# Kernel optimization log

Measured on AMD Instinct MI355X. Metric: run time of the kernel, lower is better.

Reference implementation:

```python
import jax, jax.numpy as jnp
import numpy as np

# Model constants (match init_kwargs)
B, S, H = 32, 1, 128          # batch, query seq len (decode), num query heads
SKV, G = 8192, 1              # KV cache length, KV groups (heads per group = H // G)
DIM, TAIL = 512, 64           # MLA latent (value) dim and RoPE tail dim
TOPK = 2048                   # selected KV tokens per (query, group)
KV_STRIDE = 1                 # tokens covered per KV entry
Q_START = 8191                # absolute position of the first query token
SCALE = 1.0 / np.sqrt(DIM + TAIL)  # sm_scale default: 1/sqrt(qk head dim)
NEG_INF = -1e30


def setup_inputs() -> dict:
    key = jax.random.key(0)
    kq, kkv, ki = jax.random.split(key, 3)
    Q = jax.random.normal(kq, (B, S, H, DIM + TAIL), dtype=jnp.float32)
    KV = jax.random.normal(kkv, (B, SKV, G, DIM + TAIL), dtype=jnp.float32)
    Indices = jnp.sort(
        jax.random.randint(ki, (B, S, G, TOPK), 0, SKV, dtype=jnp.int32), axis=-1)
    return {"Q": Q, "KV": KV, "Indices": Indices}


def reference(Q, KV, Indices):
    Hg = H // G  # query heads per KV group
    # Gather top-k selected KV latents: kv_sel[b,s,g,k,:] = KV[b, Indices[b,s,g,k], g, :]
    b_idx = jnp.arange(B)[:, None, None, None]
    g_idx = jnp.arange(G)[None, None, :, None]
    kv_sel = KV[b_idx, Indices, g_idx, :]               # [B, S, G, K, DIM+TAIL]
    q = Q.reshape(B, S, G, Hg, DIM + TAIL)              # group the query heads
    # Attention scores over the k selected tokens only (full dim+tail qk dot)
    scores = jnp.einsum('bsghd,bsgkd->bsghk', q, kv_sel) * SCALE
    # Causal validity: selected KV token (covering KV_STRIDE positions) must not
    # exceed the absolute query position Q_START + s.
    q_pos = Q_START + jnp.arange(S)                     # [S]
    valid = (Indices * KV_STRIDE <= q_pos[None, :, None, None]) & (Indices < SKV)
    scores = jnp.where(valid[:, :, :, None, :], scores, NEG_INF)
    p = jax.nn.softmax(scores, axis=-1)                 # [B, S, G, Hg, K]
    # Values are the first DIM channels of the latent KV (MLA: V shares latent)
    out = jnp.einsum('bsghk,bsgkd->bsghd', p, kv_sel[..., :DIM])
    return out.reshape(B, S, H, DIM)
```

## Files before the change

kernel.cpp:

```cpp
#include <hip/hip_runtime.h>
#include <hip/hip_bf16.h>

typedef short bf16x8 __attribute__((ext_vector_type(8)));
typedef float f32x4  __attribute__((ext_vector_type(4)));

#define NB    32
#define NH    128
#define DV    512
#define DQK   576
#define NKV   8192
#define NTOP  2048
#define LSTR  40
#define SCALE 0.041666666666666664f

__device__ __forceinline__ unsigned bfbits(float x) {
  union { float f; unsigned u; } c; c.f = x;
  return (c.u + 0x7FFFu + ((c.u >> 16) & 1u)) >> 16;
}
__device__ __forceinline__ unsigned pk2(float x, float y) {
  return bfbits(x) | (bfbits(y) << 16);
}
__device__ __forceinline__ short f2bf(float x) {
  return (short)bfbits(x);
}

__global__ __launch_bounds__(256) void gemm_qk(const float* __restrict__ Q, const float* __restrict__ KV,
                                               const int* __restrict__ Idx, float* __restrict__ S) {
  __shared__ short As[128 * LSTR];
  __shared__ short Bs[128 * LSTR];
  int wg = blockIdx.x;
  int b = wg >> 4, nt = wg & 15;
  int t = threadIdx.x;

  int row2 = t >> 1, half = t & 1;
  int idx = Idx[b * NTOP + nt * 128 + row2];
  const float* kvrow = KV + ((size_t)b * NKV + (size_t)idx) * DQK + half * 16;
  const float* qrow  = Q  + ((size_t)b * NH  + (size_t)row2) * DQK + half * 16;
  short* aw = &As[row2 * LSTR + half * 16];
  short* bw = &Bs[row2 * LSTR + half * 16];

  int lane = t & 63, wv = t >> 6;
  int wm = wv & 1, wn = wv >> 1;
  int m16 = lane & 15, quad = lane >> 4;

  f32x4 acc[4][4] = {};

  for (int kk = 0; kk < 18; ++kk) {
    __syncthreads();
    float4 q0 = *(const float4*)(qrow + 0);
    float4 q1 = *(const float4*)(qrow + 4);
    float4 q2 = *(const float4*)(qrow + 8);
    float4 q3 = *(const float4*)(qrow + 12);
    float4 k0 = *(const float4*)(kvrow + 0);
    float4 k1 = *(const float4*)(kvrow + 4);
    float4 k2 = *(const float4*)(kvrow + 8);
    float4 k3 = *(const float4*)(kvrow + 12);
    int4 wa0 = { (int)pk2(q0.x, q0.y), (int)pk2(q0.z, q0.w), (int)pk2(q1.x, q1.y), (int)pk2(q1.z, q1.w) };
    int4 wa1 = { (int)pk2(q2.x, q2.y), (int)pk2(q2.z, q2.w), (int)pk2(q3.x, q3.y), (int)pk2(q3.z, q3.w) };
    int4 wb0 = { (int)pk2(k0.x, k0.y), (int)pk2(k0.z, k0.w), (int)pk2(k1.x, k1.y), (int)pk2(k1.z, k1.w) };
    int4 wb1 = { (int)pk2(k2.x, k2.y), (int)pk2(k2.z, k2.w), (int)pk2(k3.x, k3.y), (int)pk2(k3.z, k3.w) };
    *(int4*)aw = wa0; *(int4*)(aw + 8) = wa1;
    *(int4*)bw = wb0; *(int4*)(bw + 8) = wb1;
    qrow += 32; kvrow += 32;
    __syncthreads();

    bf16x8 af[4], bfr[4];
#pragma unroll
    for (int i = 0; i < 4; ++i) af[i]  = *(const bf16x8*)&As[(wm * 64 + i * 16 + m16) * LSTR + quad * 8];
#pragma unroll
    for (int j = 0; j < 4; ++j) bfr[j] = *(const bf16x8*)&Bs[(wn * 64 + j * 16 + m16) * LSTR + quad * 8];
#pragma unroll
    for (int i = 0; i < 4; ++i)
#pragma unroll
      for (int j = 0; j < 4; ++j)
        acc[i][j] = __builtin_amdgcn_mfma_f32_16x16x32_bf16(af[i], bfr[j], acc[i][j], 0, 0, 0);
  }

#pragma unroll
  for (int i = 0; i < 4; ++i)
#pragma unroll
    for (int j = 0; j < 4; ++j)
#pragma unroll
      for (int r = 0; r < 4; ++r) {
        int h = wm * 64 + i * 16 + quad * 4 + r;
        int n = nt * 128 + wn * 64 + j * 16 + m16;
        S[((size_t)b * NH + h) * NTOP + n] = acc[i][j][r] * SCALE;
      }
}

__global__ __launch_bounds__(256) void softmax_k(const float* __restrict__ S, unsigned short* __restrict__ P) {
  int row = blockIdx.x;
  const float* s = S + (size_t)row * NTOP;
  unsigned short* p = P + (size_t)row * NTOP;
  int t = threadIdx.x;
  int lane = t & 63, wv = t >> 6;
  __shared__ float red[4];

  float4 v0 = *(const float4*)(s + t * 4);
  float4 v1 = *(const float4*)(s + 1024 + t * 4);

  float lm = fmaxf(fmaxf(fmaxf(v0.x, v0.y), fmaxf(v0.z, v0.w)),
                   fmaxf(fmaxf(v1.x, v1.y), fmaxf(v1.z, v1.w)));
  for (int off = 32; off > 0; off >>= 1) lm = fmaxf(lm, __shfl_down(lm, off));
  if (lane == 0) red[wv] = lm;
  __syncthreads();
  float m = fmaxf(fmaxf(red[0], red[1]), fmaxf(red[2], red[3]));

  float e0 = expf(v0.x - m), e1 = expf(v0.y - m), e2 = expf(v0.z - m), e3 = expf(v0.w - m);
  float e4 = expf(v1.x - m), e5 = expf(v1.y - m), e6 = expf(v1.z - m), e7 = expf(v1.w - m);
  float ls = ((e0 + e1) + (e2 + e3)) + ((e4 + e5) + (e6 + e7));
  for (int off = 32; off > 0; off >>= 1) ls += __shfl_down(ls, off);
  __syncthreads();
  if (lane == 0) red[wv] = ls;
  __syncthreads();
  float inv = 1.0f / (((red[0] + red[1]) + (red[2] + red[3])));

  uint2 o0 = { pk2(e0 * inv, e1 * inv), pk2(e2 * inv, e3 * inv) };
  uint2 o1 = { pk2(e4 * inv, e5 * inv), pk2(e6 * inv, e7 * inv) };
  *(uint2*)(p + t * 4) = o0;
  *(uint2*)(p + 1024 + t * 4) = o1;
}

__global__ __launch_bounds__(256) void gemm_pv(const unsigned short* __restrict__ P, const float* __restrict__ KV,
                                               const int* __restrict__ Idx, float* __restrict__ Out) {
  __shared__ short As[128 * LSTR];
  __shared__ short Bt[128 * LSTR];
  int wg = blockIdx.x;
  int b = wg >> 4, nt = (wg >> 2) & 3, ks = wg & 3;
  int t = threadIdx.x;

  int arow = t >> 1, ahalf = t & 1;
  const unsigned short* prow = P + ((size_t)b * NH + arow) * NTOP + ks * 512 + ahalf * 16;
  short* aw = &As[arow * LSTR + ahalf * 16];

  int brow = t & 31;
  int bcol = (t >> 5) * 16;
  const int* idxp = Idx + b * NTOP + ks * 512 + brow;
  short* bw = &Bt[bcol * LSTR + brow];

  int lane = t & 63, wv = t >> 6;
  int wm = wv & 1, wn = wv >> 1;
  int m16 = lane & 15, quad = lane >> 4;

  f32x4 acc[4][4] = {};

  for (int kk = 0; kk < 16; ++kk) {
    __syncthreads();
    uint4 p0 = *(const uint4*)(prow);
    uint4 p1 = *(const uint4*)(prow + 8);
    int idx = idxp[kk * 32];
    const float* vrow = KV + ((size_t)b * NKV + (size_t)idx) * DQK + nt * 128 + bcol;
    float4 v0 = *(const float4*)(vrow + 0);
    float4 v1 = *(const float4*)(vrow + 4);
    float4 v2 = *(const float4*)(vrow + 8);
    float4 v3 = *(const float4*)(vrow + 12);
    *(uint4*)aw = p0; *(uint4*)(aw + 8) = p1;
    prow += 32;
    bw[0 * LSTR]  = f2bf(v0.x); bw[1 * LSTR]  = f2bf(v0.y); bw[2 * LSTR]  = f2bf(v0.z); bw[3 * LSTR]  = f2bf(v0.w);
    bw[4 * LSTR]  = f2bf(v1.x); bw[5 * LSTR]  = f2bf(v1.y); bw[6 * LSTR]  = f2bf(v1.z); bw[7 * LSTR]  = f2bf(v1.w);
    bw[8 * LSTR]  = f2bf(v2.x); bw[9 * LSTR]  = f2bf(v2.y); bw[10 * LSTR] = f2bf(v2.z); bw[11 * LSTR] = f2bf(v2.w);
    bw[12 * LSTR] = f2bf(v3.x); bw[13 * LSTR] = f2bf(v3.y); bw[14 * LSTR] = f2bf(v3.z); bw[15 * LSTR] = f2bf(v3.w);
    __syncthreads();

    bf16x8 af[4], bfr[4];
#pragma unroll
    for (int i = 0; i < 4; ++i) af[i]  = *(const bf16x8*)&As[(wm * 64 + i * 16 + m16) * LSTR + quad * 8];
#pragma unroll
    for (int j = 0; j < 4; ++j) bfr[j] = *(const bf16x8*)&Bt[(wn * 64 + j * 16 + m16) * LSTR + quad * 8];
#pragma unroll
    for (int i = 0; i < 4; ++i)
#pragma unroll
      for (int j = 0; j < 4; ++j)
        acc[i][j] = __builtin_amdgcn_mfma_f32_16x16x32_bf16(af[i], bfr[j], acc[i][j], 0, 0, 0);
  }

#pragma unroll
  for (int i = 0; i < 4; ++i)
#pragma unroll
    for (int j = 0; j < 4; ++j)
#pragma unroll
      for (int r = 0; r < 4; ++r) {
        int h = wm * 64 + i * 16 + quad * 4 + r;
        int d = nt * 128 + wn * 64 + j * 16 + m16;
        atomicAdd(&Out[((size_t)b * NH + h) * DV + d], acc[i][j][r]);
      }
}

extern "C" void kernel_launch(void* const* d_in, const int* in_sizes, int n_in,
                              void* d_out, int out_size, void* d_ws, size_t ws_size,
                              hipStream_t stream) {
  const float* Q  = (const float*)d_in[0];
  const float* KV = (const float*)d_in[1];
  const int*  Idx = (const int*)d_in[2];

  float* S = (float*)d_ws;
  unsigned short* P = (unsigned short*)((char*)d_ws + (size_t)NB * NH * NTOP * 4);
  float* Out = (float*)d_out;

  (void)hipMemsetAsync(d_out, 0, (size_t)out_size * sizeof(float), stream);
  gemm_qk<<<dim3(NB * 16), dim3(256), 0, stream>>>(Q, KV, Idx, S);
  softmax_k<<<dim3(NB * NH), dim3(256), 0, stream>>>(S, P);
  gemm_pv<<<dim3(NB * 16), dim3(256), 0, stream>>>(P, KV, Idx, Out);
}
```

Before: 738.3 us.

## Pre-gather KV into bf16 K and transposed V, share one pipelined GEMM

Adds a gather-and-convert kernel that pulls the top-k KV rows once, converts them to bf16 and writes both a row-major K buffer and a transposed V buffer. Q is converted to bf16 separately. Both GEMMs then use a single templated bf16 NT GEMM with register prefetch of the next k-slice, replacing the fp32 loads, in-loop conversions and scalar transposed LDS stores. The PV split-K atomics are replaced by per-split partial outputs plus a reduction kernel. This adds extra workspace traffic and two more launches in exchange for contiguous, already-converted operand loads.

```diff
diff --git a/kernel.cpp b/kernel.cpp
--- a/kernel.cpp
+++ b/kernel.cpp
@@ -1,8 +1,8 @@
 #include <hip/hip_runtime.h>
-#include <hip/hip_bf16.h>
 
 typedef short bf16x8 __attribute__((ext_vector_type(8)));
 typedef float f32x4  __attribute__((ext_vector_type(4)));
+typedef unsigned short u16;
 
 #define NB    32
 #define NH    128
@@ -10,8 +10,14 @@
 #define DQK   576
 #define NKV   8192
 #define NTOP  2048
-#define LSTR  40
 #define SCALE 0.041666666666666664f
+
+#define OFF_S   0u
+#define OFF_P   33554432u
+#define OFF_QB  50331648u
+#define OFF_KB  55050240u
+#define OFF_VT  130547712u
+#define OFF_OP  197656576u
 
 __device__ __forceinline__ unsigned bfbits(float x) {
   union { float f; unsigned u; } c; c.f = x;
@@ -20,55 +26,136 @@
 __device__ __forceinline__ unsigned pk2(float x, float y) {
   return bfbits(x) | (bfbits(y) << 16);
 }
-__device__ __forceinline__ short f2bf(float x) {
-  return (short)bfbits(x);
-}
-
-__global__ __launch_bounds__(256) void gemm_qk(const float* __restrict__ Q, const float* __restrict__ KV,
-                                               const int* __restrict__ Idx, float* __restrict__ S) {
-  __shared__ short As[128 * LSTR];
-  __shared__ short Bs[128 * LSTR];
-  int wg = blockIdx.x;
-  int b = wg >> 4, nt = wg & 15;
+
+__global__ __launch_bounds__(256) void cvt_q(const float* __restrict__ Q, u16* __restrict__ Qb) {
+  int i = (blockIdx.x * 256 + threadIdx.x) * 8;
+  float4 a = *(const float4*)(Q + i), b = *(const float4*)(Q + i + 4);
+  uint4 o = { pk2(a.x, a.y), pk2(a.z, a.w), pk2(b.x, b.y), pk2(b.z, b.w) };
+  *(uint4*)(Qb + i) = o;
+}
+
+__global__ __launch_bounds__(256) void gather_cvt(const float* __restrict__ KV, const int* __restrict__ Idx,
+                                                  u16* __restrict__ Kb, u16* __restrict__ Vt) {
+  __shared__ u16 T[128 * 136];
+  int nt = blockIdx.x, b = blockIdx.y;
+  int j0 = nt * 128;
   int t = threadIdx.x;
-
-  int row2 = t >> 1, half = t & 1;
-  int idx = Idx[b * NTOP + nt * 128 + row2];
-  const float* kvrow = KV + ((size_t)b * NKV + (size_t)idx) * DQK + half * 16;
-  const float* qrow  = Q  + ((size_t)b * NH  + (size_t)row2) * DQK + half * 16;
-  short* aw = &As[row2 * LSTR + half * 16];
-  short* bw = &Bs[row2 * LSTR + half * 16];
+  const int* idxp = Idx + b * NTOP + j0;
+  const float* KVb = KV + (size_t)b * NKV * DQK;
+  u16* Kbb = Kb + ((size_t)b * NTOP + j0) * DQK;
+
+  int kq = (t & 31) * 4, dq = (t >> 5) * 16;
+  int4 id4 = *(const int4*)&idxp[kq];
+  const float* r0 = KVb + (size_t)id4.x * DQK + dq;
+  const float* r1 = KVb + (size_t)id4.y * DQK + dq;
+  const float* r2 = KVb + (size_t)id4.z * DQK + dq;
+  const float* r3 = KVb + (size_t)id4.w * DQK + dq;
+
+  int sd = t >> 1, skh = (t & 1) * 64;
+
+  for (int c = 0; c < 4; ++c) {
+    int co = c * 128;
+    unsigned rr[4][16];
+#pragma unroll
+    for (int i = 0; i < 4; ++i) {
+      const float* rp = (i == 0) ? r0 : (i == 1) ? r1 : (i == 2) ? r2 : r3;
+      float4 x0 = *(const float4*)(rp + co + 0);
+      float4 x1 = *(const float4*)(rp + co + 4);
+      float4 x2 = *(const float4*)(rp + co + 8);
+      float4 x3 = *(const float4*)(rp + co + 12);
+      rr[i][0] = bfbits(x0.x); rr[i][1] = bfbits(x0.y); rr[i][2]  = bfbits(x0.z); rr[i][3]  = bfbits(x0.w);
+      rr[i][4] = bfbits(x1.x); rr[i][5] = bfbits(x1.y); rr[i][6]  = bfbits(x1.z); rr[i][7]  = bfbits(x1.w);
+      rr[i][8] = bfbits(x2.x); rr[i][9] = bfbits(x2.y); rr[i][10] = bfbits(x2.z); rr[i][11] = bfbits(x2.w);
+      rr[i][12] = bfbits(x3.x); rr[i][13] = bfbits(x3.y); rr[i][14] = bfbits(x3.z); rr[i][15] = bfbits(x3.w);
+    }
+#pragma unroll
+    for (int i = 0; i < 4; ++i) {
+      uint4 w0 = { rr[i][0] | (rr[i][1] << 16), rr[i][2] | (rr[i][3] << 16),
+                   rr[i][4] | (rr[i][5] << 16), rr[i][6] | (rr[i][7] << 16) };
+      uint4 w1 = { rr[i][8] | (rr[i][9] << 16), rr[i][10] | (rr[i][11] << 16),
+                   rr[i][12] | (rr[i][13] << 16), rr[i][14] | (rr[i][15] << 16) };
+      u16* kp = Kbb + (size_t)(kq + i) * DQK + co + dq;
+      *(uint4*)kp = w0; *(uint4*)(kp + 8) = w1;
+    }
+#pragma unroll
+    for (int i2 = 0; i2 < 16; ++i2) {
+      uint2 w = { rr[0][i2] | (rr[1][i2] << 16), rr[2][i2] | (rr[3][i2] << 16) };
+      *(uint2*)&T[(dq + i2) * 136 + kq] = w;
+    }
+    __syncthreads();
+    u16* vp = Vt + ((size_t)b * DV + co + sd) * NTOP + j0 + skh;
+    const u16* tp = &T[sd * 136 + skh];
+#pragma unroll
+    for (int c2 = 0; c2 < 8; ++c2)
+      *(uint4*)(vp + c2 * 8) = *(const uint4*)(tp + c2 * 8);
+    __syncthreads();
+  }
+
+  int row = t >> 1, half = t & 1;
+  int idx = idxp[row];
+  const float* src = KVb + (size_t)idx * DQK + 512 + half * 32;
+  u16* dst = Kbb + (size_t)row * DQK + 512 + half * 32;
+  unsigned u[16];
+#pragma unroll
+  for (int q = 0; q < 8; ++q) {
+    float4 x = *(const float4*)(src + q * 4);
+    u[q * 2] = pk2(x.x, x.y); u[q * 2 + 1] = pk2(x.z, x.w);
+  }
+#pragma unroll
+  for (int q = 0; q < 4; ++q) {
+    uint4 w = { u[q * 4], u[q * 4 + 1], u[q * 4 + 2], u[q * 4 + 3] };
+    *(uint4*)(dst + q * 8) = w;
+  }
+}
+
+template <int NKI, int LD>
+__global__ __launch_bounds__(256) void gemm_nt(const u16* __restrict__ A, const u16* __restrict__ B,
+                                               float* __restrict__ C, int ldc,
+                                               int aB, int bB, int bT, int cB, int cT, int cK, int KS,
+                                               float scale) {
+  __shared__ u16 As[128 * 32];
+  __shared__ u16 Bs[128 * 32];
+  int nt = blockIdx.x, b = blockIdx.y, ks = blockIdx.z;
+  const u16* Ab = A + (size_t)b * aB + (size_t)ks * KS;
+  const u16* Bb = B + (size_t)b * bB + (size_t)nt * bT + (size_t)ks * KS;
+  float* Cb = C + (size_t)b * cB + (size_t)nt * cT + (size_t)ks * cK;
+
+  int t = threadIdx.x;
+  int r0 = t >> 2, kq = (t & 3) * 8;
+  const u16* ag = Ab + (size_t)r0 * LD + kq;
+  const u16* bg = Bb + (size_t)r0 * LD + kq;
+  u16* aw = &As[r0 * 32 + kq];
+  u16* bw = &Bs[r0 * 32 + kq];
 
   int lane = t & 63, wv = t >> 6;
   int wm = wv & 1, wn = wv >> 1;
   int m16 = lane & 15, quad = lane >> 4;
 
+  uint4 ra0 = *(const uint4*)(ag);
+  uint4 ra1 = *(const uint4*)(ag + (size_t)64 * LD);
+  uint4 rb0 = *(const uint4*)(bg);
+  uint4 rb1 = *(const uint4*)(bg + (size_t)64 * LD);
+
   f32x4 acc[4][4] = {};
 
-  for (int kk = 0; kk < 18; ++kk) {
-    __syncthreads();
-    float4 q0 = *(const float4*)(qrow + 0);
-    float4 q1 = *(const float4*)(qrow + 4);
-    float4 q2 = *(const float4*)(qrow + 8);
-    float4 q3 = *(const float4*)(qrow + 12);
-    float4 k0 = *(const float4*)(kvrow + 0);
-    float4 k1 = *(const float4*)(kvrow + 4);
-    float4 k2 = *(const float4*)(kvrow + 8);
-    float4 k3 = *(const float4*)(kvrow + 12);
-    int4 wa0 = { (int)pk2(q0.x, q0.y), (int)pk2(q0.z, q0.w), (int)pk2(q1.x, q1.y), (int)pk2(q1.z, q1.w) };
-    int4 wa1 = { (int)pk2(q2.x, q2.y), (int)pk2(q2.z, q2.w), (int)pk2(q3.x, q3.y), (int)pk2(q3.z, q3.w) };
-    int4 wb0 = { (int)pk2(k0.x, k0.y), (int)pk2(k0.z, k0.w), (int)pk2(k1.x, k1.y), (int)pk2(k1.z, k1.w) };
-    int4 wb1 = { (int)pk2(k2.x, k2.y), (int)pk2(k2.z, k2.w), (int)pk2(k3.x, k3.y), (int)pk2(k3.z, k3.w) };
-    *(int4*)aw = wa0; *(int4*)(aw + 8) = wa1;
-    *(int4*)bw = wb0; *(int4*)(bw + 8) = wb1;
-    qrow += 32; kvrow += 32;
-    __syncthreads();
-
+  for (int kk = 0; kk < NKI; ++kk) {
+    __syncthreads();
+    *(uint4*)aw = ra0; *(uint4*)(aw + 64 * 32) = ra1;
+    *(uint4*)bw = rb0; *(uint4*)(bw + 64 * 32) = rb1;
+    __syncthreads();
+    if (kk + 1 < NKI) {
+      const u16* an = ag + (kk + 1) * 32;
+      const u16* bn = bg + (kk + 1) * 32;
+      ra0 = *(const uint4*)(an);
+      ra1 = *(const uint4*)(an + (size_t)64 * LD);
+      rb0 = *(const uint4*)(bn);
+      rb1 = *(const uint4*)(bn + (size_t)64 * LD);
+    }
     bf16x8 af[4], bfr[4];
 #pragma unroll
-    for (int i = 0; i < 4; ++i) af[i]  = *(const bf16x8*)&As[(wm * 64 + i * 16 + m16) * LSTR + quad * 8];
-#pragma unroll
-    for (int j = 0; j < 4; ++j) bfr[j] = *(const bf16x8*)&Bs[(wn * 64 + j * 16 + m16) * LSTR + quad * 8];
+    for (int i = 0; i < 4; ++i) af[i]  = *(const bf16x8*)&As[(wm * 64 + i * 16 + m16) * 32 + quad * 8];
+#pragma unroll
+    for (int j = 0; j < 4; ++j) bfr[j] = *(const bf16x8*)&Bs[(wn * 64 + j * 16 + m16) * 32 + quad * 8];
 #pragma unroll
     for (int i = 0; i < 4; ++i)
 #pragma unroll
@@ -82,16 +169,16 @@
     for (int j = 0; j < 4; ++j)
 #pragma unroll
       for (int r = 0; r < 4; ++r) {
-        int h = wm * 64 + i * 16 + quad * 4 + r;
-        int n = nt * 128 + wn * 64 + j * 16 + m16;
-        S[((size_t)b * NH + h) * NTOP + n] = acc[i][j][r] * SCALE;
+        int m = wm * 64 + i * 16 + quad * 4 + r;
+        int n = wn * 64 + j * 16 + m16;
+        Cb[(size_t)m * ldc + n] = acc[i][j][r] * scale;
       }
 }
 
-__global__ __launch_bounds__(256) void softmax_k(const float* __restrict__ S, unsigned short* __restrict__ P) {
+__global__ __launch_bounds__(256) void softmax_k(const float* __restrict__ S, u16* __restrict__ P) {
   int row = blockIdx.x;
   const float* s = S + (size_t)row * NTOP;
-  unsigned short* p = P + (size_t)row * NTOP;
+  u16* p = P + (size_t)row * NTOP;
   int t = threadIdx.x;
   int lane = t & 63, wv = t >> 6;
   __shared__ float red[4];
@@ -121,69 +208,16 @@
   *(uint2*)(p + 1024 + t * 4) = o1;
 }
 
-__global__ __launch_bounds__(256) void gemm_pv(const unsigned short* __restrict__ P, const float* __restrict__ KV,
-                                               const int* __restrict__ Idx, float* __restrict__ Out) {
-  __shared__ short As[128 * LSTR];
-  __shared__ short Bt[128 * LSTR];
-  int wg = blockIdx.x;
-  int b = wg >> 4, nt = (wg >> 2) & 3, ks = wg & 3;
-  int t = threadIdx.x;
-
-  int arow = t >> 1, ahalf = t & 1;
-  const unsigned short* prow = P + ((size_t)b * NH + arow) * NTOP + ks * 512 + ahalf * 16;
-  short* aw = &As[arow * LSTR + ahalf * 16];
-
-  int brow = t & 31;
-  int bcol = (t >> 5) * 16;
-  const int* idxp = Idx + b * NTOP + ks * 512 + brow;
-  short* bw = &Bt[bcol * LSTR + brow];
-
-  int lane = t & 63, wv = t >> 6;
-  int wm = wv & 1, wn = wv >> 1;
-  int m16 = lane & 15, quad = lane >> 4;
-
-  f32x4 acc[4][4] = {};
-
-  for (int kk = 0; kk < 16; ++kk) {
-    __syncthreads();
-    uint4 p0 = *(const uint4*)(prow);
-    uint4 p1 = *(const uint4*)(prow + 8);
-    int idx = idxp[kk * 32];
-    const float* vrow = KV + ((size_t)b * NKV + (size_t)idx) * DQK + nt * 128 + bcol;
-    float4 v0 = *(const float4*)(vrow + 0);
-    float4 v1 = *(const float4*)(vrow + 4);
-    float4 v2 = *(const float4*)(vrow + 8);
-    float4 v3 = *(const float4*)(vrow + 12);
-    *(uint4*)aw = p0; *(uint4*)(aw + 8) = p1;
-    prow += 32;
-    bw[0 * LSTR]  = f2bf(v0.x); bw[1 * LSTR]  = f2bf(v0.y); bw[2 * LSTR]  = f2bf(v0.z); bw[3 * LSTR]  = f2bf(v0.w);
-    bw[4 * LSTR]  = f2bf(v1.x); bw[5 * LSTR]  = f2bf(v1.y); bw[6 * LSTR]  = f2bf(v1.z); bw[7 * LSTR]  = f2bf(v1.w);
-    bw[8 * LSTR]  = f2bf(v2.x); bw[9 * LSTR]  = f2bf(v2.y); bw[10 * LSTR] = f2bf(v2.z); bw[11 * LSTR] = f2bf(v2.w);
-    bw[12 * LSTR] = f2bf(v3.x); bw[13 * LSTR] = f2bf(v3.y); bw[14 * LSTR] = f2bf(v3.z); bw[15 * LSTR] = f2bf(v3.w);
-    __syncthreads();
-
-    bf16x8 af[4], bfr[4];
-#pragma unroll
-    for (int i = 0; i < 4; ++i) af[i]  = *(const bf16x8*)&As[(wm * 64 + i * 16 + m16) * LSTR + quad * 8];
-#pragma unroll
-    for (int j = 0; j < 4; ++j) bfr[j] = *(const bf16x8*)&Bt[(wn * 64 + j * 16 + m16) * LSTR + quad * 8];
-#pragma unroll
-    for (int i = 0; i < 4; ++i)
-#pragma unroll
-      for (int j = 0; j < 4; ++j)
-        acc[i][j] = __builtin_amdgcn_mfma_f32_16x16x32_bf16(af[i], bfr[j], acc[i][j], 0, 0, 0);
-  }
-
-#pragma unroll
-  for (int i = 0; i < 4; ++i)
-#pragma unroll
-    for (int j = 0; j < 4; ++j)
-#pragma unroll
-      for (int r = 0; r < 4; ++r) {
-        int h = wm * 64 + i * 16 + quad * 4 + r;
-        int d = nt * 128 + wn * 64 + j * 16 + m16;
-        atomicAdd(&Out[((size_t)b * NH + h) * DV + d], acc[i][j][r]);
-      }
+__global__ __launch_bounds__(256) void reduce4(const float* __restrict__ Op, float* __restrict__ Out) {
+  size_t i = ((size_t)blockIdx.x * 256 + threadIdx.x) * 4;
+  const size_t STRIDE = (size_t)NB * NH * DV;
+  float4 s0 = *(const float4*)(Op + i);
+  float4 s1 = *(const float4*)(Op + STRIDE + i);
+  float4 s2 = *(const float4*)(Op + 2 * STRIDE + i);
+  float4 s3 = *(const float4*)(Op + 3 * STRIDE + i);
+  float4 o = { (s0.x + s1.x) + (s2.x + s3.x), (s0.y + s1.y) + (s2.y + s3.y),
+               (s0.z + s1.z) + (s2.z + s3.z), (s0.w + s1.w) + (s2.w + s3.w) };
+  *(float4*)(Out + i) = o;
 }
 
 extern "C" void kernel_launch(void* const* d_in, const int* in_sizes, int n_in,
@@ -193,12 +227,25 @@
   const float* KV = (const float*)d_in[1];
   const int*  Idx = (const int*)d_in[2];
 
-  float* S = (float*)d_ws;
-  unsigned short* P = (unsigned short*)((char*)d_ws + (size_t)NB * NH * NTOP * 4);
+  char* ws = (char*)d_ws;
+  float* S   = (float*)(ws + OFF_S);
+  u16*   P   = (u16*)(ws + OFF_P);
+  u16*   Qb  = (u16*)(ws + OFF_QB);
+  u16*   Kb  = (u16*)(ws + OFF_KB);
+  u16*   Vt  = (u16*)(ws + OFF_VT);
+  float* Op  = (float*)(ws + OFF_OP);
   float* Out = (float*)d_out;
 
-  (void)hipMemsetAsync(d_out, 0, (size_t)out_size * sizeof(float), stream);
-  gemm_qk<<<dim3(NB * 16), dim3(256), 0, stream>>>(Q, KV, Idx, S);
+  cvt_q<<<dim3(1152), dim3(256), 0, stream>>>(Q, Qb);
+  gather_cvt<<<dim3(16, 32), dim3(256), 0, stream>>>(KV, Idx, Kb, Vt);
+  gemm_nt<18, 576><<<dim3(16, 32, 1), dim3(256), 0, stream>>>(
+      Qb, Kb, S, NTOP,
+       NH * DQK,  NTOP * DQK,  128 * DQK,
+       NH * NTOP,  128,  0,  0, SCALE);
   softmax_k<<<dim3(NB * NH), dim3(256), 0, stream>>>(S, P);
-  gemm_pv<<<dim3(NB * 16), dim3(256), 0, stream>>>(P, KV, Idx, Out);
-}
+  gemm_nt<16, 2048><<<dim3(4, 32, 4), dim3(256), 0, stream>>>(
+      P, Vt, Op, DV,
+       NH * NTOP,  DV * NTOP,  128 * NTOP,
+       NH * DV,  128,  NB * NH * DV,  512, 1.0f);
+  reduce4<<<dim3(2048), dim3(256), 0, stream>>>(Op, Out);
+}
```

Measured after the change: 788.7 us. 1.07x slower.

## Fuse QK, softmax and PV into split-K flash kernel with combine pass

Applied to the files above, without the earlier changes.

Replaces the three-kernel pipeline (QK GEMM to a global score matrix, separate softmax, PV GEMM with atomics) with one split-K flash-style kernel. Each block handles 128 selected keys: it computes scores, takes a local max/sum softmax into shared memory, and multiplies by gathered V, writing partial outputs plus row max and sum. A second kernel rescales and combines the 16 partials. This removes the fp32 score and P round-trips, the memset and the atomics, and adds register prefetch of the next QK tile and a swizzled V layout. In exchange it writes a large fp32 partial-output buffer (16x the output size) and adds a combine pass.

```diff
diff --git a/kernel.cpp b/kernel.cpp
--- a/kernel.cpp
+++ b/kernel.cpp
@@ -1,8 +1,8 @@
 #include <hip/hip_runtime.h>
-#include <hip/hip_bf16.h>
 
 typedef short bf16x8 __attribute__((ext_vector_type(8)));
 typedef float f32x4  __attribute__((ext_vector_type(4)));
+typedef unsigned short u16;
 
 #define NB    32
 #define NH    128
@@ -10,8 +10,14 @@
 #define DQK   576
 #define NKV   8192
 #define NTOP  2048
-#define LSTR  40
+#define NCH   16
+#define KC    128
+#define PSTR  136
 #define SCALE 0.041666666666666664f
+
+#define OFF_OP 0u
+#define OFF_M  134217728u
+#define OFF_L  134479872u
 
 __device__ __forceinline__ unsigned bfbits(float x) {
   union { float f; unsigned u; } c; c.f = x;
@@ -20,170 +26,245 @@
 __device__ __forceinline__ unsigned pk2(float x, float y) {
   return bfbits(x) | (bfbits(y) << 16);
 }
-__device__ __forceinline__ short f2bf(float x) {
-  return (short)bfbits(x);
-}
-
-__global__ __launch_bounds__(256) void gemm_qk(const float* __restrict__ Q, const float* __restrict__ KV,
-                                               const int* __restrict__ Idx, float* __restrict__ S) {
-  __shared__ short As[128 * LSTR];
-  __shared__ short Bs[128 * LSTR];
-  int wg = blockIdx.x;
-  int b = wg >> 4, nt = wg & 15;
+
+__global__ __launch_bounds__(256) void flash_chunk(const float* __restrict__ Q, const float* __restrict__ KV,
+                                                   const int* __restrict__ Idx,
+                                                   float* __restrict__ Op, float* __restrict__ Mg,
+                                                   float* __restrict__ Lg) {
+  __shared__ u16 Psh[128 * PSTR];
+  __shared__ u16 U[8192];
+  __shared__ float Msh[2 * 128];
+  __shared__ float Lsh[2 * 128];
+
+  u16* As = U;
+  u16* Bs = U + 4096;
+  u16* Vt = U;
+
+  int blk = blockIdx.x;
+  int b = blk >> 4, ks = blk & 15;
   int t = threadIdx.x;
-
-  int row2 = t >> 1, half = t & 1;
-  int idx = Idx[b * NTOP + nt * 128 + row2];
-  const float* kvrow = KV + ((size_t)b * NKV + (size_t)idx) * DQK + half * 16;
-  const float* qrow  = Q  + ((size_t)b * NH  + (size_t)row2) * DQK + half * 16;
-  short* aw = &As[row2 * LSTR + half * 16];
-  short* bw = &Bs[row2 * LSTR + half * 16];
-
   int lane = t & 63, wv = t >> 6;
   int wm = wv & 1, wn = wv >> 1;
   int m16 = lane & 15, quad = lane >> 4;
 
+  const float* Qb  = Q  + (size_t)b * NH * DQK;
+  const float* KVb = KV + (size_t)b * NKV * DQK;
+  const int* idxp  = Idx + b * NTOP + ks * KC;
+
+  int sr = t >> 1, sh = (t & 1) * 16;
+  int bidx = idxp[sr];
+  const float* aq = Qb + (size_t)sr * DQK + sh;
+  const float* bk = KVb + (size_t)bidx * DQK + sh;
+  u16* aw = &As[sr * 32 + sh];
+  u16* bw = &Bs[sr * 32 + sh];
+
   f32x4 acc[4][4] = {};
+
+  float4 a0 = *(const float4*)(aq);
+  float4 a1 = *(const float4*)(aq + 4);
+  float4 a2 = *(const float4*)(aq + 8);
+  float4 a3 = *(const float4*)(aq + 12);
+  float4 b0 = *(const float4*)(bk);
+  float4 b1 = *(const float4*)(bk + 4);
+  float4 b2 = *(const float4*)(bk + 8);
+  float4 b3 = *(const float4*)(bk + 12);
 
   for (int kk = 0; kk < 18; ++kk) {
     __syncthreads();
-    float4 q0 = *(const float4*)(qrow + 0);
-    float4 q1 = *(const float4*)(qrow + 4);
-    float4 q2 = *(const float4*)(qrow + 8);
-    float4 q3 = *(const float4*)(qrow + 12);
-    float4 k0 = *(const float4*)(kvrow + 0);
-    float4 k1 = *(const float4*)(kvrow + 4);
-    float4 k2 = *(const float4*)(kvrow + 8);
-    float4 k3 = *(const float4*)(kvrow + 12);
-    int4 wa0 = { (int)pk2(q0.x, q0.y), (int)pk2(q0.z, q0.w), (int)pk2(q1.x, q1.y), (int)pk2(q1.z, q1.w) };
-    int4 wa1 = { (int)pk2(q2.x, q2.y), (int)pk2(q2.z, q2.w), (int)pk2(q3.x, q3.y), (int)pk2(q3.z, q3.w) };
-    int4 wb0 = { (int)pk2(k0.x, k0.y), (int)pk2(k0.z, k0.w), (int)pk2(k1.x, k1.y), (int)pk2(k1.z, k1.w) };
-    int4 wb1 = { (int)pk2(k2.x, k2.y), (int)pk2(k2.z, k2.w), (int)pk2(k3.x, k3.y), (int)pk2(k3.z, k3.w) };
-    *(int4*)aw = wa0; *(int4*)(aw + 8) = wa1;
-    *(int4*)bw = wb0; *(int4*)(bw + 8) = wb1;
-    qrow += 32; kvrow += 32;
+    {
+      uint4 wa0 = { pk2(a0.x, a0.y), pk2(a0.z, a0.w), pk2(a1.x, a1.y), pk2(a1.z, a1.w) };
+      uint4 wa1 = { pk2(a2.x, a2.y), pk2(a2.z, a2.w), pk2(a3.x, a3.y), pk2(a3.z, a3.w) };
+      uint4 wb0 = { pk2(b0.x, b0.y), pk2(b0.z, b0.w), pk2(b1.x, b1.y), pk2(b1.z, b1.w) };
+      uint4 wb1 = { pk2(b2.x, b2.y), pk2(b2.z, b2.w), pk2(b3.x, b3.y), pk2(b3.z, b3.w) };
+      *(uint4*)aw = wa0; *(uint4*)(aw + 8) = wa1;
+      *(uint4*)bw = wb0; *(uint4*)(bw + 8) = wb1;
+    }
     __syncthreads();
-
-    bf16x8 af[4], bfr[4];
-#pragma unroll
-    for (int i = 0; i < 4; ++i) af[i]  = *(const bf16x8*)&As[(wm * 64 + i * 16 + m16) * LSTR + quad * 8];
-#pragma unroll
-    for (int j = 0; j < 4; ++j) bfr[j] = *(const bf16x8*)&Bs[(wn * 64 + j * 16 + m16) * LSTR + quad * 8];
+    if (kk + 1 < 18) {
+      const float* an = aq + (kk + 1) * 32;
+      const float* bn = bk + (kk + 1) * 32;
+      a0 = *(const float4*)(an);     a1 = *(const float4*)(an + 4);
+      a2 = *(const float4*)(an + 8); a3 = *(const float4*)(an + 12);
+      b0 = *(const float4*)(bn);     b1 = *(const float4*)(bn + 4);
+      b2 = *(const float4*)(bn + 8); b3 = *(const float4*)(bn + 12);
+    }
+    bf16x8 af[4], bf[4];
+#pragma unroll
+    for (int i = 0; i < 4; ++i) af[i] = *(const bf16x8*)&As[(wm * 64 + i * 16 + m16) * 32 + quad * 8];
+#pragma unroll
+    for (int j = 0; j < 4; ++j) bf[j] = *(const bf16x8*)&Bs[(wn * 64 + j * 16 + m16) * 32 + quad * 8];
 #pragma unroll
     for (int i = 0; i < 4; ++i)
 #pragma unroll
       for (int j = 0; j < 4; ++j)
-        acc[i][j] = __builtin_amdgcn_mfma_f32_16x16x32_bf16(af[i], bfr[j], acc[i][j], 0, 0, 0);
+        acc[i][j] = __builtin_amdgcn_mfma_f32_16x16x32_bf16(af[i], bf[j], acc[i][j], 0, 0, 0);
   }
 
 #pragma unroll
   for (int i = 0; i < 4; ++i)
 #pragma unroll
     for (int j = 0; j < 4; ++j)
+      acc[i][j] *= SCALE;
+
+  float mx[4][4];
+#pragma unroll
+  for (int i = 0; i < 4; ++i)
+#pragma unroll
+    for (int r = 0; r < 4; ++r) {
+      float v = fmaxf(fmaxf(acc[i][0][r], acc[i][1][r]), fmaxf(acc[i][2][r], acc[i][3][r]));
+      v = fmaxf(v, __shfl_xor(v, 1)); v = fmaxf(v, __shfl_xor(v, 2));
+      v = fmaxf(v, __shfl_xor(v, 4)); v = fmaxf(v, __shfl_xor(v, 8));
+      mx[i][r] = v;
+    }
+  if (m16 == 0) {
+#pragma unroll
+    for (int i = 0; i < 4; ++i)
+#pragma unroll
+      for (int r = 0; r < 4; ++r)
+        Msh[wn * 128 + wm * 64 + i * 16 + quad * 4 + r] = mx[i][r];
+  }
+  __syncthreads();
+  float mrw[4][4];
+#pragma unroll
+  for (int i = 0; i < 4; ++i)
+#pragma unroll
+    for (int r = 0; r < 4; ++r) {
+      int row = wm * 64 + i * 16 + quad * 4 + r;
+      mrw[i][r] = fmaxf(Msh[row], Msh[128 + row]);
+    }
+  float sm[4][4];
+#pragma unroll
+  for (int i = 0; i < 4; ++i)
+#pragma unroll
+    for (int r = 0; r < 4; ++r) {
+      float s = 0.f;
+#pragma unroll
+      for (int j = 0; j < 4; ++j) {
+        float e = expf(acc[i][j][r] - mrw[i][r]);
+        acc[i][j][r] = e;
+        s += e;
+      }
+      s += __shfl_xor(s, 1); s += __shfl_xor(s, 2);
+      s += __shfl_xor(s, 4); s += __shfl_xor(s, 8);
+      sm[i][r] = s;
+    }
+  if (m16 == 0) {
+#pragma unroll
+    for (int i = 0; i < 4; ++i)
+#pragma unroll
+      for (int r = 0; r < 4; ++r)
+        Lsh[wn * 128 + wm * 64 + i * 16 + quad * 4 + r] = sm[i][r];
+  }
+#pragma unroll
+  for (int i = 0; i < 4; ++i)
+#pragma unroll
+    for (int j = 0; j < 4; ++j)
 #pragma unroll
       for (int r = 0; r < 4; ++r) {
-        int h = wm * 64 + i * 16 + quad * 4 + r;
-        int n = nt * 128 + wn * 64 + j * 16 + m16;
-        S[((size_t)b * NH + h) * NTOP + n] = acc[i][j][r] * SCALE;
-      }
-}
-
-__global__ __launch_bounds__(256) void softmax_k(const float* __restrict__ S, unsigned short* __restrict__ P) {
+        int row = wm * 64 + i * 16 + quad * 4 + r;
+        int col = wn * 64 + j * 16 + m16;
+        Psh[row * PSTR + col] = (u16)bfbits(acc[i][j][r]);
+      }
+  __syncthreads();
+  if (wn == 0 && m16 == 0) {
+    float* mg = Mg + (b * NCH + ks) * NH;
+    float* lg = Lg + (b * NCH + ks) * NH;
+#pragma unroll
+    for (int i = 0; i < 4; ++i)
+#pragma unroll
+      for (int r = 0; r < 4; ++r) {
+        int row = wm * 64 + i * 16 + quad * 4 + r;
+        mg[row] = mrw[i][r];
+        lg[row] = Lsh[row] + Lsh[128 + row];
+      }
+  }
+
+  int p  = t & 15;
+  int dg = t >> 4;
+  float* opb = Op + (((size_t)ks * NB + b) * NH) * DV;
+
+  for (int dh = 0; dh < 4; ++dh) {
+    f32x4 a4[4][4] = {};
+    for (int k2 = 0; k2 < 4; ++k2) {
+      int key0 = k2 * 32 + p * 2;
+      int i0 = idxp[key0], i1 = idxp[key0 + 1];
+      const float* v0p = KVb + (size_t)i0 * DQK + dh * 128 + dg * 8;
+      const float* v1p = KVb + (size_t)i1 * DQK + dh * 128 + dg * 8;
+      float4 x0 = *(const float4*)(v0p);
+      float4 x1 = *(const float4*)(v0p + 4);
+      float4 y0 = *(const float4*)(v1p);
+      float4 y1 = *(const float4*)(v1p + 4);
+      unsigned lo[8] = { bfbits(x0.x), bfbits(x0.y), bfbits(x0.z), bfbits(x0.w),
+                         bfbits(x1.x), bfbits(x1.y), bfbits(x1.z), bfbits(x1.w) };
+      unsigned hi[8] = { bfbits(y0.x), bfbits(y0.y), bfbits(y0.z), bfbits(y0.w),
+                         bfbits(y1.x), bfbits(y1.y), bfbits(y1.z), bfbits(y1.w) };
+      __syncthreads();
+      int chunk = (p >> 2) ^ (dg & 3);
+#pragma unroll
+      for (int jj = 0; jj < 8; ++jj) {
+        int row = dg * 8 + jj;
+        int elem = row * 32 + chunk * 8 + (p & 3) * 2;
+        *(unsigned*)&Vt[elem] = lo[jj] | (hi[jj] << 16);
+      }
+      __syncthreads();
+      bf16x8 af2[4], bf2[4];
+#pragma unroll
+      for (int i = 0; i < 4; ++i)
+        af2[i] = *(const bf16x8*)&Psh[(wm * 64 + i * 16 + m16) * PSTR + k2 * 32 + quad * 8];
+#pragma unroll
+      for (int j = 0; j < 4; ++j) {
+        int row = wn * 64 + j * 16 + m16;
+        int rchunk = quad ^ ((row >> 3) & 3);
+        bf2[j] = *(const bf16x8*)&Vt[row * 32 + rchunk * 8];
+      }
+#pragma unroll
+      for (int i = 0; i < 4; ++i)
+#pragma unroll
+        for (int j = 0; j < 4; ++j)
+          a4[i][j] = __builtin_amdgcn_mfma_f32_16x16x32_bf16(af2[i], bf2[j], a4[i][j], 0, 0, 0);
+    }
+#pragma unroll
+    for (int i = 0; i < 4; ++i)
+#pragma unroll
+      for (int j = 0; j < 4; ++j)
+#pragma unroll
+        for (int r = 0; r < 4; ++r) {
+          int h = wm * 64 + i * 16 + quad * 4 + r;
+          int d = dh * 128 + wn * 64 + j * 16 + m16;
+          opb[(size_t)h * DV + d] = a4[i][j][r];
+        }
+  }
+}
+
+__global__ __launch_bounds__(256) void combine(const float* __restrict__ Op, const float* __restrict__ Mg,
+                                               const float* __restrict__ Lg, float* __restrict__ Out) {
   int row = blockIdx.x;
-  const float* s = S + (size_t)row * NTOP;
-  unsigned short* p = P + (size_t)row * NTOP;
+  int b = row >> 7, h = row & 127;
   int t = threadIdx.x;
-  int lane = t & 63, wv = t >> 6;
-  __shared__ float red[4];
-
-  float4 v0 = *(const float4*)(s + t * 4);
-  float4 v1 = *(const float4*)(s + 1024 + t * 4);
-
-  float lm = fmaxf(fmaxf(fmaxf(v0.x, v0.y), fmaxf(v0.z, v0.w)),
-                   fmaxf(fmaxf(v1.x, v1.y), fmaxf(v1.z, v1.w)));
-  for (int off = 32; off > 0; off >>= 1) lm = fmaxf(lm, __shfl_down(lm, off));
-  if (lane == 0) red[wv] = lm;
-  __syncthreads();
-  float m = fmaxf(fmaxf(red[0], red[1]), fmaxf(red[2], red[3]));
-
-  float e0 = expf(v0.x - m), e1 = expf(v0.y - m), e2 = expf(v0.z - m), e3 = expf(v0.w - m);
-  float e4 = expf(v1.x - m), e5 = expf(v1.y - m), e6 = expf(v1.z - m), e7 = expf(v1.w - m);
-  float ls = ((e0 + e1) + (e2 + e3)) + ((e4 + e5) + (e6 + e7));
-  for (int off = 32; off > 0; off >>= 1) ls += __shfl_down(ls, off);
-  __syncthreads();
-  if (lane == 0) red[wv] = ls;
-  __syncthreads();
-  float inv = 1.0f / (((red[0] + red[1]) + (red[2] + red[3])));
-
-  uint2 o0 = { pk2(e0 * inv, e1 * inv), pk2(e2 * inv, e3 * inv) };
-  uint2 o1 = { pk2(e4 * inv, e5 * inv), pk2(e6 * inv, e7 * inv) };
-  *(uint2*)(p + t * 4) = o0;
-  *(uint2*)(p + 1024 + t * 4) = o1;
-}
-
-__global__ __launch_bounds__(256) void gemm_pv(const unsigned short* __restrict__ P, const float* __restrict__ KV,
-                                               const int* __restrict__ Idx, float* __restrict__ Out) {
-  __shared__ short As[128 * LSTR];
-  __shared__ short Bt[128 * LSTR];
-  int wg = blockIdx.x;
-  int b = wg >> 4, nt = (wg >> 2) & 3, ks = wg & 3;
-  int t = threadIdx.x;
-
-  int arow = t >> 1, ahalf = t & 1;
-  const unsigned short* prow = P + ((size_t)b * NH + arow) * NTOP + ks * 512 + ahalf * 16;
-  short* aw = &As[arow * LSTR + ahalf * 16];
-
-  int brow = t & 31;
-  int bcol = (t >> 5) * 16;
-  const int* idxp = Idx + b * NTOP + ks * 512 + brow;
-  short* bw = &Bt[bcol * LSTR + brow];
-
-  int lane = t & 63, wv = t >> 6;
-  int wm = wv & 1, wn = wv >> 1;
-  int m16 = lane & 15, quad = lane >> 4;
-
-  f32x4 acc[4][4] = {};
-
-  for (int kk = 0; kk < 16; ++kk) {
-    __syncthreads();
-    uint4 p0 = *(const uint4*)(prow);
-    uint4 p1 = *(const uint4*)(prow + 8);
-    int idx = idxp[kk * 32];
-    const float* vrow = KV + ((size_t)b * NKV + (size_t)idx) * DQK + nt * 128 + bcol;
-    float4 v0 = *(const float4*)(vrow + 0);
-    float4 v1 = *(const float4*)(vrow + 4);
-    float4 v2 = *(const float4*)(vrow + 8);
-    float4 v3 = *(const float4*)(vrow + 12);
-    *(uint4*)aw = p0; *(uint4*)(aw + 8) = p1;
-    prow += 32;
-    bw[0 * LSTR]  = f2bf(v0.x); bw[1 * LSTR]  = f2bf(v0.y); bw[2 * LSTR]  = f2bf(v0.z); bw[3 * LSTR]  = f2bf(v0.w);
-    bw[4 * LSTR]  = f2bf(v1.x); bw[5 * LSTR]  = f2bf(v1.y); bw[6 * LSTR]  = f2bf(v1.z); bw[7 * LSTR]  = f2bf(v1.w);
-    bw[8 * LSTR]  = f2bf(v2.x); bw[9 * LSTR]  = f2bf(v2.y); bw[10 * LSTR] = f2bf(v2.z); bw[11 * LSTR] = f2bf(v2.w);
-    bw[12 * LSTR] = f2bf(v3.x); bw[13 * LSTR] = f2bf(v3.y); bw[14 * LSTR] = f2bf(v3.z); bw[15 * LSTR] = f2bf(v3.w);
-    __syncthreads();
-
-    bf16x8 af[4], bfr[4];
-#pragma unroll
-    for (int i = 0; i < 4; ++i) af[i]  = *(const bf16x8*)&As[(wm * 64 + i * 16 + m16) * LSTR + quad * 8];
-#pragma unroll
-    for (int j = 0; j < 4; ++j) bfr[j] = *(const bf16x8*)&Bt[(wn * 64 + j * 16 + m16) * LSTR + quad * 8];
-#pragma unroll
-    for (int i = 0; i < 4; ++i)
-#pragma unroll
-      for (int j = 0; j < 4; ++j)
-        acc[i][j] = __builtin_amdgcn_mfma_f32_16x16x32_bf16(af[i], bfr[j], acc[i][j], 0, 0, 0);
-  }
-
-#pragma unroll
-  for (int i = 0; i < 4; ++i)
-#pragma unroll
-    for (int j = 0; j < 4; ++j)
-#pragma unroll
-      for (int r = 0; r < 4; ++r) {
-        int h = wm * 64 + i * 16 + quad * 4 + r;
-        int d = nt * 128 + wn * 64 + j * 16 + m16;
-        atomicAdd(&Out[((size_t)b * NH + h) * DV + d], acc[i][j][r]);
-      }
+
+  float m[NCH], l[NCH];
+#pragma unroll
+  for (int c = 0; c < NCH; ++c) {
+    m[c] = Mg[(b * NCH + c) * NH + h];
+    l[c] = Lg[(b * NCH + c) * NH + h];
+  }
+  float M = m[0];
+#pragma unroll
+  for (int c = 1; c < NCH; ++c) M = fmaxf(M, m[c]);
+  float L = 0.f, w[NCH];
+#pragma unroll
+  for (int c = 0; c < NCH; ++c) { w[c] = expf(m[c] - M); L += l[c] * w[c]; }
+  float inv = 1.0f / L;
+
+  float ox = 0.f, oy = 0.f;
+#pragma unroll
+  for (int c = 0; c < NCH; ++c) {
+    const float* src = Op + (((size_t)c * NB + b) * NH + h) * DV + t * 2;
+    float2 v = *(const float2*)src;
+    ox += w[c] * v.x; oy += w[c] * v.y;
+  }
+  float2 o = { ox * inv, oy * inv };
+  *(float2*)(Out + ((size_t)b * NH + h) * DV + t * 2) = o;
 }
 
 extern "C" void kernel_launch(void* const* d_in, const int* in_sizes, int n_in,
@@ -193,12 +274,12 @@
   const float* KV = (const float*)d_in[1];
   const int*  Idx = (const int*)d_in[2];
 
-  float* S = (float*)d_ws;
-  unsigned short* P = (unsigned short*)((char*)d_ws + (size_t)NB * NH * NTOP * 4);
+  char* ws = (char*)d_ws;
+  float* Op = (float*)(ws + OFF_OP);
+  float* Mg = (float*)(ws + OFF_M);
+  float* Lg = (float*)(ws + OFF_L);
   float* Out = (float*)d_out;
 
-  (void)hipMemsetAsync(d_out, 0, (size_t)out_size * sizeof(float), stream);
-  gemm_qk<<<dim3(NB * 16), dim3(256), 0, stream>>>(Q, KV, Idx, S);
-  softmax_k<<<dim3(NB * NH), dim3(256), 0, stream>>>(S, P);
-  gemm_pv<<<dim3(NB * 16), dim3(256), 0, stream>>>(P, KV, Idx, Out);
-}
+  flash_chunk<<<dim3(NB * NCH), dim3(256), 0, stream>>>(Q, KV, Idx, Op, Mg, Lg);
+  combine<<<dim3(NB * NH), dim3(256), 0, stream>>>(Op, Mg, Lg, Out);
+}
```

Measured after the change: 757.2 us. 1.03x slower.
